# Kernel optimization log

Measured on AMD Instinct MI355X. Metric: run time of the kernel, lower is better.

The kernel has to match this reference:

```python
import jax, jax.numpy as jnp
import numpy as np

D_MODEL = 1024
N_HEADS = 16
HEAD_DIM = D_MODEL // N_HEADS


def setup_inputs() -> dict:
    key = jax.random.key(0)
    ks = jax.random.split(key, 5)
    x = jax.random.normal(ks[0], (4, 2048, D_MODEL), dtype=jnp.float32)
    # qkv Linear: weight [3*d_model, d_model], bias [3*d_model]
    w_qkv = jax.random.normal(ks[1], (3 * D_MODEL, D_MODEL), dtype=jnp.float32) / np.sqrt(D_MODEL)
    b_qkv = jnp.zeros((3 * D_MODEL,), dtype=jnp.float32)
    w_out = jax.random.normal(ks[2], (D_MODEL, D_MODEL), dtype=jnp.float32) / np.sqrt(D_MODEL)
    b_out = jnp.zeros((D_MODEL,), dtype=jnp.float32)
    return {"x": x, "w_qkv": w_qkv, "b_qkv": b_qkv, "w_out": w_out, "b_out": b_out}


def reference(x, w_qkv, b_qkv, w_out, b_out):
    B, T, C = x.shape
    H, Dh = N_HEADS, HEAD_DIM
    qkv = x @ w_qkv.T + b_qkv                      # [B,T,3C]
    qkv = qkv.reshape(B, T, 3, H, Dh)
    q = jnp.transpose(qkv[:, :, 0], (0, 2, 1, 3))  # [B,H,T,Dh]
    k = jnp.transpose(qkv[:, :, 1], (0, 2, 1, 3))
    v = jnpp_transpose = jnp.transpose(qkv[:, :, 2], (0, 2, 1, 3))
    scale = 1.0 / np.sqrt(Dh).astype(np.float32)
    att = jnp.einsum('bhqd,bhkd->bhqk', q, k) * scale
    causal = jnp.tril(jnp.ones((T, T), dtype=bool))
    att = jnp.where(causal[None, None], att, -jnp.inf)
    att = jax.nn.softmax(att, axis=-1)
    head_out = jnp.einsum('bhqk,bhkd->bhqd', att, v)  # [B,H,T,Dh]
    out = jnp.transpose(head_out, (0, 2, 1, 3)).reshape(B, T, C)
    return out @ w_out.T + b_out
```

## Files before the change

### kernel.cpp

```cpp
#include <hip/hip_runtime.h>
#include <hip/hip_bf16.h>


#define D_MODEL 1024
#define N_HEADS 16
#define HEAD_DIM 64
#define SEQ 2048
#define BATCH 4

typedef __attribute__((ext_vector_type(8))) short bf16x8;
typedef __attribute__((ext_vector_type(4))) float f32x4;
typedef unsigned int uint;

__device__ __forceinline__ short f2bf(float f) {
    union { float f; uint i; } c; c.f = f;
    uint x = c.i;
    x += 0x7fffu + ((x >> 16) & 1u);
    return (short)(x >> 16);
}
__device__ __forceinline__ uint pack2(float a, float b) {
    return (uint)(unsigned short)f2bf(a) | ((uint)(unsigned short)f2bf(b) << 16);
}
__device__ __forceinline__ uint asu(float f) { union { float f; uint i; } c; c.f = f; return c.i; }
__device__ __forceinline__ uint packtr(float lo, float hi) {
    return __builtin_amdgcn_perm(asu(hi), asu(lo), 0x07060302u);
}

__device__ __forceinline__ void glds16(const void* g, void* l) {
    __builtin_amdgcn_global_load_lds(
        (const __attribute__((address_space(1))) uint*)g,
        (__attribute__((address_space(3))) uint*)l, 16, 0, 0);
}

__global__ __launch_bounds__(256) void cvt3_bf16(const float* __restrict__ s0,
                                                 const float* __restrict__ s1,
                                                 const float* __restrict__ s2,
                                                 short* __restrict__ dst,
                                                 int n0, int n01) {
    int i = blockIdx.x * 256 + threadIdx.x;
    const float* src;
    int off;
    if (i < n0)       { src = s0; off = i; }
    else if (i < n01) { src = s1; off = i - n0; }
    else              { src = s2; off = i - n01; }
    float4 f = *(const float4*)(src + (size_t)off * 4);
    uint2 o; o.x = pack2(f.x, f.y); o.y = pack2(f.z, f.w);
    *(uint2*)(dst + (size_t)i * 4) = o;
}

template <int MODE>
__global__ __launch_bounds__(256, 2) void gemm_bt(
    const short* __restrict__ A, const short* __restrict__ B,
    const float* __restrict__ bias, float* __restrict__ Cp,
    int M, int N, int K,
    short* __restrict__ qp, short* __restrict__ kp, short* __restrict__ vp)
{
    __shared__ short As[128][32];
    __shared__ short Bs[128][32];
    const int tid = threadIdx.x;
    const int wave = tid >> 6, lane = tid & 63;
    const int quad = lane >> 4, l16 = lane & 15;
    const int wm = (wave >> 1) * 64, wn = (wave & 1) * 64;
    const int rowBase = blockIdx.y * 128;
    const int colBase = blockIdx.x * 128;

    const short* gA = A + (size_t)(rowBase + wave * 32 + (lane >> 2)) * K + (lane & 3) * 8;
    const short* gB = B + (size_t)(colBase + wave * 32 + (lane >> 2)) * K + (lane & 3) * 8;
    void* lA0 = &As[wave * 32][0];
    void* lA1 = &As[wave * 32 + 16][0];
    void* lB0 = &Bs[wave * 32][0];
    void* lB1 = &Bs[wave * 32 + 16][0];

    f32x4 acc[4][4] = {};

    for (int k0 = 0; k0 < K; k0 += 32) {
        __syncthreads();
        glds16(gA + k0, lA0);
        glds16(gA + (size_t)16 * K + k0, lA1);
        glds16(gB + k0, lB0);
        glds16(gB + (size_t)16 * K + k0, lB1);
        __syncthreads();
        bf16x8 af[4], bfr[4];
#pragma unroll
        for (int i = 0; i < 4; ++i)
            af[i] = *(const bf16x8*)&As[wm + i * 16 + l16][quad * 8];
#pragma unroll
        for (int j = 0; j < 4; ++j)
            bfr[j] = *(const bf16x8*)&Bs[wn + j * 16 + l16][quad * 8];
#pragma unroll
        for (int i = 0; i < 4; ++i)
#pragma unroll
            for (int j = 0; j < 4; ++j)
                acc[i][j] = __builtin_amdgcn_mfma_f32_16x16x32_bf16(af[i], bfr[j], acc[i][j], 0, 0, 0);
    }

#pragma unroll
    for (int i = 0; i < 4; ++i) {
#pragma unroll
        for (int j = 0; j < 4; ++j) {
#pragma unroll
            for (int r = 0; r < 4; ++r) {
                int row = rowBase + wm + i * 16 + quad * 4 + r;
                int col = colBase + wn + j * 16 + l16;
                float v = acc[i][j][r] + bias[col];
                if (MODE == 0) {
                    Cp[(size_t)row * N + col] = v;
                } else {
                    int which = col >> 10;
                    int h = (col >> 6) & 15;
                    int d = col & 63;
                    int b = row >> 11;
                    int t = row & 2047;
                    short* dst = (which == 0) ? qp : (which == 1) ? kp : vp;
                    dst[((((size_t)b * N_HEADS + h) * SEQ) + t) * HEAD_DIM + d] = f2bf(v);
                }
            }
        }
    }
}

__global__ __launch_bounds__(256, 2) void attn_fwd(
    const short* __restrict__ Q, const short* __restrict__ K,
    const short* __restrict__ V, short* __restrict__ O)
{
    __shared__ short Ks[64][72];
    __shared__ short Vt[64][72];
    __shared__ short Ps[128][72];
    const int tid = threadIdx.x;
    const int wave = tid >> 6, lane = tid & 63;
    const int quad = lane >> 4, l16 = lane & 15;
    const int bh = blockIdx.x;
    const int b = bh >> 4, h = bh & 15;
    const int qt = gridDim.y - 1 - blockIdx.y;
    const int qbase = qt * 128;
    const short* Qh = Q + (size_t)bh * SEQ * HEAD_DIM;
    const short* Kh = K + (size_t)bh * SEQ * HEAD_DIM;
    const short* Vh = V + (size_t)bh * SEQ * HEAD_DIM;

    const float C1 = 0.125f * 1.44269504f;
    const float C2 = 14.4269504f;

    bf16x8 onesf;
#pragma unroll
    for (int e = 0; e < 8; ++e) onesf[e] = (short)0x3F80;

    bf16x8 qf[2][2];
#pragma unroll
    for (int m = 0; m < 2; ++m)
#pragma unroll
        for (int st = 0; st < 2; ++st)
            qf[m][st] = *(const bf16x8*)(Qh + (size_t)(qbase + wave * 32 + m * 16 + l16) * HEAD_DIM + st * 32 + quad * 8);

    f32x4 o[2][4] = {};
    f32x4 osum[2] = {};

    const int subw = qbase + wave * 32;
    const int subS = __builtin_amdgcn_readfirstlane(subw);

    const int kr = tid >> 2, kc = (tid & 3) * 16;
    const int vk = (tid & 31) * 2, vd = (tid >> 5) * 8;

    const int ntiles = 2 * qt + 2;
    int4 kv0 = *(const int4*)(Kh + (size_t)kr * HEAD_DIM + kc);
    int4 kv1 = *(const int4*)(Kh + (size_t)kr * HEAD_DIM + kc + 8);
    int4 vv0 = *(const int4*)(Vh + (size_t)vk * HEAD_DIM + vd);
    int4 vv1 = *(const int4*)(Vh + (size_t)(vk + 1) * HEAD_DIM + vd);

    for (int j = 0; j < ntiles; ++j) {
        const int kb = j * 64;
        __syncthreads();
        *(int4*)&Ks[kr][kc] = kv0;
        *(int4*)&Ks[kr][kc + 8] = kv1;
        {
            const uint* pa = (const uint*)&vv0;
            const uint* pb = (const uint*)&vv1;
#pragma unroll
            for (int e = 0; e < 4; ++e) {
                uint lo = __builtin_amdgcn_perm(pb[e], pa[e], 0x05040100u);
                uint hi = __builtin_amdgcn_perm(pb[e], pa[e], 0x07060302u);
                *(uint*)&Vt[vd + 2 * e][vk] = lo;
                *(uint*)&Vt[vd + 2 * e + 1][vk] = hi;
            }
        }
        __syncthreads();

        {
            const int kbn = (j + 1 < ntiles) ? kb + 64 : kb;
            kv0 = *(const int4*)(Kh + (size_t)(kbn + kr) * HEAD_DIM + kc);
            kv1 = *(const int4*)(Kh + (size_t)(kbn + kr) * HEAD_DIM + kc + 8);
            vv0 = *(const int4*)(Vh + (size_t)(kbn + vk) * HEAD_DIM + vd);
            vv1 = *(const int4*)(Vh + (size_t)(kbn + vk + 1) * HEAD_DIM + vd);
        }

        if (kb > subS + 31) continue;

        {
            const int prowb = wave * 32 + l16;
#pragma unroll
            for (int kt = 0; kt < 4; ++kt) {
                const int kbkt = kb + kt * 16;
                bf16x8 kf0, kf1;
                if (kbkt <= subS + 31) {
                    kf0 = *(const bf16x8*)&Ks[kt * 16 + l16][quad * 8];
                    kf1 = *(const bf16x8*)&Ks[kt * 16 + l16][32 + quad * 8];
                }
#pragma unroll
                for (int m = 0; m < 2; ++m) {
                    const int sub = subS + m * 16;
                    uint2 u;
                    if (kbkt > sub + 15) {
                        u.x = 0u; u.y = 0u;
                    } else {
                        f32x4 tt = {0.f, 0.f, 0.f, 0.f};
                        tt = __builtin_amdgcn_mfma_f32_16x16x32_bf16(kf0, qf[m][0], tt, 0, 0, 0);
                        tt = __builtin_amdgcn_mfma_f32_16x16x32_bf16(kf1, qf[m][1], tt, 0, 0, 0);
                        float p[4];
                        if (kbkt + 15 <= sub) {
#pragma unroll
                            for (int r = 0; r < 4; ++r)
                                p[r] = __builtin_exp2f(__builtin_fmaf(tt[r], C1, -C2));
                        } else {
                            const int qrow = sub + l16;
#pragma unroll
                            for (int r = 0; r < 4; ++r) {
                                float a = __builtin_fmaf(tt[r], C1, -C2);
                                if (kbkt + quad * 4 + r > qrow) a = -1e30f;
                                p[r] = __builtin_exp2f(a);
                            }
                        }
                        u.x = packtr(p[0], p[1]); u.y = packtr(p[2], p[3]);
                    }
                    *(uint2*)&Ps[prowb + m * 16][kt * 16 + quad * 4] = u;
                }
            }
        }
#pragma unroll
        for (int st = 0; st < 2; ++st) {
            if (st == 1 && kb + 32 > subS + 31) break;
            bf16x8 pf0 = *(const bf16x8*)&Ps[wave * 32 + l16][st * 32 + quad * 8];
            bf16x8 pf1 = *(const bf16x8*)&Ps[wave * 32 + 16 + l16][st * 32 + quad * 8];
            osum[0] = __builtin_amdgcn_mfma_f32_16x16x32_bf16(pf0, onesf, osum[0], 0, 0, 0);
            osum[1] = __builtin_amdgcn_mfma_f32_16x16x32_bf16(pf1, onesf, osum[1], 0, 0, 0);
#pragma unroll
            for (int dt = 0; dt < 4; ++dt) {
                bf16x8 vf = *(const bf16x8*)&Vt[dt * 16 + l16][st * 32 + quad * 8];
                o[0][dt] = __builtin_amdgcn_mfma_f32_16x16x32_bf16(pf0, vf, o[0][dt], 0, 0, 0);
                o[1][dt] = __builtin_amdgcn_mfma_f32_16x16x32_bf16(pf1, vf, o[1][dt], 0, 0, 0);
            }
        }
    }

#pragma unroll
    for (int m = 0; m < 2; ++m) {
#pragma unroll
        for (int r = 0; r < 4; ++r) {
            float inv = 1.f / osum[m][r];
            int t = qbase + wave * 32 + m * 16 + quad * 4 + r;
            size_t base = ((size_t)b * SEQ + t) * D_MODEL + h * HEAD_DIM;
#pragma unroll
            for (int dt = 0; dt < 4; ++dt)
                O[base + dt * 16 + l16] = f2bf(o[m][dt][r] * inv);
        }
    }
}

extern "C" void kernel_launch(void* const* d_in, const int* in_sizes, int n_in,
                              void* d_out, int out_size, void* d_ws, size_t ws_size,
                              hipStream_t stream)
{
    const float* x     = (const float*)d_in[0];
    const float* w_qkv = (const float*)d_in[1];
    const float* b_qkv = (const float*)d_in[2];
    const float* w_out = (const float*)d_in[3];
    const float* b_out = (const float*)d_in[4];
    float* out = (float*)d_out;

    const int NX = BATCH * SEQ * D_MODEL;
    const int NWQ = 3 * D_MODEL * D_MODEL;
    const int NWO = D_MODEL * D_MODEL;
    const size_t HE = (size_t)BATCH * N_HEADS * SEQ * HEAD_DIM;

    short* xb    = (short*)d_ws;
    short* wqkvb = xb + NX;
    short* woutb = wqkvb + NWQ;
    short* qp    = woutb + NWO;
    short* kp    = qp + HE;
    short* vp    = kp + HE;
    short* ho    = xb;

    const int M = BATCH * SEQ;

    cvt3_bf16<<<(NX + NWQ + NWO) / 1024, 256, 0, stream>>>(
        x, w_qkv, w_out, xb, NX / 4, (NX + NWQ) / 4);

    gemm_bt<1><<<dim3(3 * D_MODEL / 128, M / 128), 256, 0, stream>>>(
        xb, wqkvb, b_qkv, nullptr, M, 3 * D_MODEL, D_MODEL, qp, kp, vp);

    attn_fwd<<<dim3(BATCH * N_HEADS, SEQ / 128), 256, 0, stream>>>(qp, kp, vp, ho);

    gemm_bt<0><<<dim3(D_MODEL / 128, M / 128), 256, 0, stream>>>(
        ho, woutb, b_out, out, M, D_MODEL, D_MODEL, nullptr, nullptr, nullptr);
}
```

Before: 253.4 us.

## Rewrite GEMM as 256x256 tile with double-buffered async LDS prefetch

Replaces the 128x128 single-buffered GEMM with a 256x256, 512-thread kernel using a K-step of 64. Two LDS buffers are filled by direct global-to-LDS loads so the next tile is fetched while MFMAs run, with vmcnt waits and raised wave priority during the MFMA bursts. The larger tile raises reuse per loaded byte and the double buffering hides load latency. The cost is 128 KB of LDS per block and fewer blocks: the QKV GEMM gets 384 blocks, but the output projection only 128, which leaves some CUs idle on the 256-CU part.

Result: slower. 294.1 us (+16.1%).

```diff
diff --git a/kernel.cpp b/kernel.cpp
--- a/kernel.cpp
+++ b/kernel.cpp
@@ -49,60 +49,98 @@
 }
 
 template <int MODE>
-__global__ __launch_bounds__(256, 2) void gemm_bt(
+__global__ __launch_bounds__(512, 2) void gemm256(
     const short* __restrict__ A, const short* __restrict__ B,
     const float* __restrict__ bias, float* __restrict__ Cp,
     int M, int N, int K,
     short* __restrict__ qp, short* __restrict__ kp, short* __restrict__ vp)
 {
-    __shared__ short As[128][32];
-    __shared__ short Bs[128][32];
+    __shared__ short As[2][256][64];
+    __shared__ short Bs[2][256][64];
     const int tid = threadIdx.x;
-    const int wave = tid >> 6, lane = tid & 63;
+    const int lane = tid & 63;
+    const int wid = tid >> 6;
+    const int wr = wid >> 2, wc = wid & 3;
     const int quad = lane >> 4, l16 = lane & 15;
-    const int wm = (wave >> 1) * 64, wn = (wave & 1) * 64;
-    const int rowBase = blockIdx.y * 128;
-    const int colBase = blockIdx.x * 128;
-
-    const short* gA = A + (size_t)(rowBase + wave * 32 + (lane >> 2)) * K + (lane & 3) * 8;
-    const short* gB = B + (size_t)(colBase + wave * 32 + (lane >> 2)) * K + (lane & 3) * 8;
-    void* lA0 = &As[wave * 32][0];
-    void* lA1 = &As[wave * 32 + 16][0];
-    void* lB0 = &Bs[wave * 32][0];
-    void* lB1 = &Bs[wave * 32 + 16][0];
-
-    f32x4 acc[4][4] = {};
-
-    for (int k0 = 0; k0 < K; k0 += 32) {
-        __syncthreads();
-        glds16(gA + k0, lA0);
-        glds16(gA + (size_t)16 * K + k0, lA1);
-        glds16(gB + k0, lB0);
-        glds16(gB + (size_t)16 * K + k0, lB1);
-        __syncthreads();
-        bf16x8 af[4], bfr[4];
-#pragma unroll
-        for (int i = 0; i < 4; ++i)
-            af[i] = *(const bf16x8*)&As[wm + i * 16 + l16][quad * 8];
-#pragma unroll
-        for (int j = 0; j < 4; ++j)
-            bfr[j] = *(const bf16x8*)&Bs[wn + j * 16 + l16][quad * 8];
-#pragma unroll
-        for (int i = 0; i < 4; ++i)
-#pragma unroll
-            for (int j = 0; j < 4; ++j)
-                acc[i][j] = __builtin_amdgcn_mfma_f32_16x16x32_bf16(af[i], bfr[j], acc[i][j], 0, 0, 0);
-    }
-
-#pragma unroll
-    for (int i = 0; i < 4; ++i) {
-#pragma unroll
-        for (int j = 0; j < 4; ++j) {
+    const int rowBase = blockIdx.y * 256;
+    const int colBase = blockIdx.x * 256;
+
+    const int srow = tid >> 3;
+    const int scol = (tid & 7) * 8;
+    const short* gA = A + (size_t)(rowBase + srow) * K + scol;
+    const short* gB = B + (size_t)(colBase + srow) * K + scol;
+    const int ldsrow = wid << 3;
+
+    f32x4 acc[8][4] = {};
+    const int NT = K / 64;
+
+#define STAGE(buf, t)                                                         \
+    {                                                                         \
+        const int k0_ = (t) * 64;                                             \
+        _Pragma("unroll")                                                     \
+        for (int i_ = 0; i_ < 4; ++i_)                                        \
+            glds16(gA + (size_t)(i_ * 64) * K + k0_,                          \
+                   &As[buf][i_ * 64 + ldsrow][0]);                            \
+        _Pragma("unroll")                                                     \
+        for (int i_ = 0; i_ < 4; ++i_)                                        \
+            glds16(gB + (size_t)(i_ * 64) * K + k0_,                          \
+                   &Bs[buf][i_ * 64 + ldsrow][0]);                            \
+    }
+
+    STAGE(0, 0)
+    STAGE(1, 1)
+    int cur = 0;
+
+    for (int t = 0; t < NT; ++t) {
+        if (t + 1 < NT) asm volatile("s_waitcnt vmcnt(8)" ::: "memory");
+        else            asm volatile("s_waitcnt vmcnt(0)" ::: "memory");
+        __builtin_amdgcn_s_barrier();
+        __builtin_amdgcn_sched_barrier(0);
+
+        bf16x8 bfr[4][2];
+#pragma unroll
+        for (int ni = 0; ni < 4; ++ni)
+#pragma unroll
+            for (int ks = 0; ks < 2; ++ks)
+                bfr[ni][ks] = *(const bf16x8*)&Bs[cur][wc * 64 + ni * 16 + l16][ks * 32 + quad * 8];
+
+#pragma unroll
+        for (int half = 0; half < 2; ++half) {
+            bf16x8 af[4][2];
+#pragma unroll
+            for (int mi = 0; mi < 4; ++mi)
+#pragma unroll
+                for (int ks = 0; ks < 2; ++ks)
+                    af[mi][ks] = *(const bf16x8*)&As[cur][wr * 128 + half * 64 + mi * 16 + l16][ks * 32 + quad * 8];
+            __builtin_amdgcn_s_setprio(1);
+#pragma unroll
+            for (int mi = 0; mi < 4; ++mi)
+#pragma unroll
+                for (int ni = 0; ni < 4; ++ni) {
+                    acc[half * 4 + mi][ni] = __builtin_amdgcn_mfma_f32_16x16x32_bf16(
+                        af[mi][0], bfr[ni][0], acc[half * 4 + mi][ni], 0, 0, 0);
+                    acc[half * 4 + mi][ni] = __builtin_amdgcn_mfma_f32_16x16x32_bf16(
+                        af[mi][1], bfr[ni][1], acc[half * 4 + mi][ni], 0, 0, 0);
+                }
+            __builtin_amdgcn_s_setprio(0);
+        }
+
+        __builtin_amdgcn_s_barrier();
+        __builtin_amdgcn_sched_barrier(0);
+        if (t + 2 < NT) STAGE(cur, t + 2)
+        cur ^= 1;
+    }
+#undef STAGE
+
+#pragma unroll
+    for (int mi = 0; mi < 8; ++mi) {
+#pragma unroll
+        for (int ni = 0; ni < 4; ++ni) {
 #pragma unroll
             for (int r = 0; r < 4; ++r) {
-                int row = rowBase + wm + i * 16 + quad * 4 + r;
-                int col = colBase + wn + j * 16 + l16;
-                float v = acc[i][j][r] + bias[col];
+                int row = rowBase + wr * 128 + mi * 16 + quad * 4 + r;
+                int col = colBase + wc * 64 + ni * 16 + l16;
+                float v = acc[mi][ni][r] + bias[col];
                 if (MODE == 0) {
                     Cp[(size_t)row * N + col] = v;
                 } else {
@@ -110,9 +148,9 @@
                     int h = (col >> 6) & 15;
                     int d = col & 63;
                     int b = row >> 11;
-                    int t = row & 2047;
+                    int t2 = row & 2047;
                     short* dst = (which == 0) ? qp : (which == 1) ? kp : vp;
-                    dst[((((size_t)b * N_HEADS + h) * SEQ) + t) * HEAD_DIM + d] = f2bf(v);
+                    dst[((((size_t)b * N_HEADS + h) * SEQ) + t2) * HEAD_DIM + d] = f2bf(v);
                 }
             }
         }
@@ -293,11 +331,11 @@
     cvt3_bf16<<<(NX + NWQ + NWO) / 1024, 256, 0, stream>>>(
         x, w_qkv, w_out, xb, NX / 4, (NX + NWQ) / 4);
 
-    gemm_bt<1><<<dim3(3 * D_MODEL / 128, M / 128), 256, 0, stream>>>(
+    gemm256<1><<<dim3(3 * D_MODEL / 256, M / 256), 512, 0, stream>>>(
         xb, wqkvb, b_qkv, nullptr, M, 3 * D_MODEL, D_MODEL, qp, kp, vp);
 
     attn_fwd<<<dim3(BATCH * N_HEADS, SEQ / 128), 256, 0, stream>>>(qp, kp, vp, ho);
 
-    gemm_bt<0><<<dim3(D_MODEL / 128, M / 128), 256, 0, stream>>>(
+    gemm256<0><<<dim3(D_MODEL / 256, M / 256), 512, 0, stream>>>(
         ho, woutb, b_out, out, M, D_MODEL, D_MODEL, nullptr, nullptr, nullptr);
 }
```

## Double-buffer LDS tiles in GEMM and attention and raise MFMA wave priority

Applied to the files above, without the earlier changes.

The GEMM now stages the next K-slice into a second LDS buffer while MFMAs run on the current one, leaving one barrier per iteration instead of two. The attention kernel double-buffers the K and transposed V tiles so the barrier before each tile's LDS writes can be dropped. It also wraps the PV MFMA block in s_setprio so waves issuing matrix ops get scheduling priority. The cost is double the LDS for these tiles, which may limit occupancy, and correctness now depends on the async LDS loads being complete by the single barrier.

New measurement: 261.4 us. +3.2%, slower.

```diff
diff --git a/kernel.cpp b/kernel.cpp
--- a/kernel.cpp
+++ b/kernel.cpp
@@ -55,8 +55,8 @@
     int M, int N, int K,
     short* __restrict__ qp, short* __restrict__ kp, short* __restrict__ vp)
 {
-    __shared__ short As[128][32];
-    __shared__ short Bs[128][32];
+    __shared__ short As[2][128][32];
+    __shared__ short Bs[2][128][32];
     const int tid = threadIdx.x;
     const int wave = tid >> 6, lane = tid & 63;
     const int quad = lane >> 4, l16 = lane & 15;
@@ -66,33 +66,39 @@
 
     const short* gA = A + (size_t)(rowBase + wave * 32 + (lane >> 2)) * K + (lane & 3) * 8;
     const short* gB = B + (size_t)(colBase + wave * 32 + (lane >> 2)) * K + (lane & 3) * 8;
-    void* lA0 = &As[wave * 32][0];
-    void* lA1 = &As[wave * 32 + 16][0];
-    void* lB0 = &Bs[wave * 32][0];
-    void* lB1 = &Bs[wave * 32 + 16][0];
 
     f32x4 acc[4][4] = {};
-
-    for (int k0 = 0; k0 < K; k0 += 32) {
-        __syncthreads();
-        glds16(gA + k0, lA0);
-        glds16(gA + (size_t)16 * K + k0, lA1);
-        glds16(gB + k0, lB0);
-        glds16(gB + (size_t)16 * K + k0, lB1);
-        __syncthreads();
+    const int NT = K / 32;
+
+#define GSTAGE(buf, k0)                                                \
+    {                                                                  \
+        glds16(gA + (k0), &As[buf][wave * 32][0]);                     \
+        glds16(gA + (size_t)16 * K + (k0), &As[buf][wave * 32 + 16][0]); \
+        glds16(gB + (k0), &Bs[buf][wave * 32][0]);                     \
+        glds16(gB + (size_t)16 * K + (k0), &Bs[buf][wave * 32 + 16][0]); \
+    }
+
+    GSTAGE(0, 0)
+    __syncthreads();
+
+    for (int t = 0; t < NT; ++t) {
+        const int cur = t & 1;
+        if (t + 1 < NT) GSTAGE(cur ^ 1, (t + 1) * 32)
         bf16x8 af[4], bfr[4];
 #pragma unroll
         for (int i = 0; i < 4; ++i)
-            af[i] = *(const bf16x8*)&As[wm + i * 16 + l16][quad * 8];
+            af[i] = *(const bf16x8*)&As[cur][wm + i * 16 + l16][quad * 8];
 #pragma unroll
         for (int j = 0; j < 4; ++j)
-            bfr[j] = *(const bf16x8*)&Bs[wn + j * 16 + l16][quad * 8];
+            bfr[j] = *(const bf16x8*)&Bs[cur][wn + j * 16 + l16][quad * 8];
 #pragma unroll
         for (int i = 0; i < 4; ++i)
 #pragma unroll
             for (int j = 0; j < 4; ++j)
                 acc[i][j] = __builtin_amdgcn_mfma_f32_16x16x32_bf16(af[i], bfr[j], acc[i][j], 0, 0, 0);
-    }
+        __syncthreads();
+    }
+#undef GSTAGE
 
 #pragma unroll
     for (int i = 0; i < 4; ++i) {
@@ -110,9 +116,9 @@
                     int h = (col >> 6) & 15;
                     int d = col & 63;
                     int b = row >> 11;
-                    int t = row & 2047;
+                    int t2 = row & 2047;
                     short* dst = (which == 0) ? qp : (which == 1) ? kp : vp;
-                    dst[((((size_t)b * N_HEADS + h) * SEQ) + t) * HEAD_DIM + d] = f2bf(v);
+                    dst[((((size_t)b * N_HEADS + h) * SEQ) + t2) * HEAD_DIM + d] = f2bf(v);
                 }
             }
         }
@@ -123,8 +129,8 @@
     const short* __restrict__ Q, const short* __restrict__ K,
     const short* __restrict__ V, short* __restrict__ O)
 {
-    __shared__ short Ks[64][72];
-    __shared__ short Vt[64][72];
+    __shared__ short Ks[2][64][72];
+    __shared__ short Vt[2][64][72];
     __shared__ short Ps[128][72];
     const int tid = threadIdx.x;
     const int wave = tid >> 6, lane = tid & 63;
@@ -168,9 +174,9 @@
 
     for (int j = 0; j < ntiles; ++j) {
         const int kb = j * 64;
-        __syncthreads();
-        *(int4*)&Ks[kr][kc] = kv0;
-        *(int4*)&Ks[kr][kc + 8] = kv1;
+        const int p = j & 1;
+        *(int4*)&Ks[p][kr][kc] = kv0;
+        *(int4*)&Ks[p][kr][kc + 8] = kv1;
         {
             const uint* pa = (const uint*)&vv0;
             const uint* pb = (const uint*)&vv1;
@@ -178,19 +184,18 @@
             for (int e = 0; e < 4; ++e) {
                 uint lo = __builtin_amdgcn_perm(pb[e], pa[e], 0x05040100u);
                 uint hi = __builtin_amdgcn_perm(pb[e], pa[e], 0x07060302u);
-                *(uint*)&Vt[vd + 2 * e][vk] = lo;
-                *(uint*)&Vt[vd + 2 * e + 1][vk] = hi;
+                *(uint*)&Vt[p][vd + 2 * e][vk] = lo;
+                *(uint*)&Vt[p][vd + 2 * e + 1][vk] = hi;
             }
         }
-        __syncthreads();
-
-        {
-            const int kbn = (j + 1 < ntiles) ? kb + 64 : kb;
+        if (j + 1 < ntiles) {
+            const int kbn = kb + 64;
             kv0 = *(const int4*)(Kh + (size_t)(kbn + kr) * HEAD_DIM + kc);
             kv1 = *(const int4*)(Kh + (size_t)(kbn + kr) * HEAD_DIM + kc + 8);
             vv0 = *(const int4*)(Vh + (size_t)(kbn + vk) * HEAD_DIM + vd);
             vv1 = *(const int4*)(Vh + (size_t)(kbn + vk + 1) * HEAD_DIM + vd);
         }
+        __syncthreads();
 
         if (kb > subS + 31) continue;
 
@@ -201,8 +206,8 @@
                 const int kbkt = kb + kt * 16;
                 bf16x8 kf0, kf1;
                 if (kbkt <= subS + 31) {
-                    kf0 = *(const bf16x8*)&Ks[kt * 16 + l16][quad * 8];
-                    kf1 = *(const bf16x8*)&Ks[kt * 16 + l16][32 + quad * 8];
+                    kf0 = *(const bf16x8*)&Ks[p][kt * 16 + l16][quad * 8];
+                    kf1 = *(const bf16x8*)&Ks[p][kt * 16 + l16][32 + quad * 8];
                 }
 #pragma unroll
                 for (int m = 0; m < 2; ++m) {
@@ -214,21 +219,21 @@
                         f32x4 tt = {0.f, 0.f, 0.f, 0.f};
                         tt = __builtin_amdgcn_mfma_f32_16x16x32_bf16(kf0, qf[m][0], tt, 0, 0, 0);
                         tt = __builtin_amdgcn_mfma_f32_16x16x32_bf16(kf1, qf[m][1], tt, 0, 0, 0);
-                        float p[4];
+                        float pp[4];
                         if (kbkt + 15 <= sub) {
 #pragma unroll
                             for (int r = 0; r < 4; ++r)
-                                p[r] = __builtin_exp2f(__builtin_fmaf(tt[r], C1, -C2));
+                                pp[r] = __builtin_exp2f(__builtin_fmaf(tt[r], C1, -C2));
                         } else {
                             const int qrow = sub + l16;
 #pragma unroll
                             for (int r = 0; r < 4; ++r) {
                                 float a = __builtin_fmaf(tt[r], C1, -C2);
                                 if (kbkt + quad * 4 + r > qrow) a = -1e30f;
-                                p[r] = __builtin_exp2f(a);
+                                pp[r] = __builtin_exp2f(a);
                             }
                         }
-                        u.x = packtr(p[0], p[1]); u.y = packtr(p[2], p[3]);
+                        u.x = packtr(pp[0], pp[1]); u.y = packtr(pp[2], pp[3]);
                     }
                     *(uint2*)&Ps[prowb + m * 16][kt * 16 + quad * 4] = u;
                 }
@@ -239,14 +244,16 @@
             if (st == 1 && kb + 32 > subS + 31) break;
             bf16x8 pf0 = *(const bf16x8*)&Ps[wave * 32 + l16][st * 32 + quad * 8];
             bf16x8 pf1 = *(const bf16x8*)&Ps[wave * 32 + 16 + l16][st * 32 + quad * 8];
+            __builtin_amdgcn_s_setprio(1);
             osum[0] = __builtin_amdgcn_mfma_f32_16x16x32_bf16(pf0, onesf, osum[0], 0, 0, 0);
             osum[1] = __builtin_amdgcn_mfma_f32_16x16x32_bf16(pf1, onesf, osum[1], 0, 0, 0);
 #pragma unroll
             for (int dt = 0; dt < 4; ++dt) {
-                bf16x8 vf = *(const bf16x8*)&Vt[dt * 16 + l16][st * 32 + quad * 8];
+                bf16x8 vf = *(const bf16x8*)&Vt[p][dt * 16 + l16][st * 32 + quad * 8];
                 o[0][dt] = __builtin_amdgcn_mfma_f32_16x16x32_bf16(pf0, vf, o[0][dt], 0, 0, 0);
                 o[1][dt] = __builtin_amdgcn_mfma_f32_16x16x32_bf16(pf1, vf, o[1][dt], 0, 0, 0);
             }
+            __builtin_amdgcn_s_setprio(0);
         }
     }
 
```
